# Optimization experiments

Measured on AMD Instinct MI355X. Metric: run time of the kernel, lower is better.

The kernel has to match this reference:

```python
import jax, jax.numpy as jnp
import numpy as np

EMBED = 1024

def setup_inputs() -> dict:
    key = jax.random.key(0)
    kx, kq, kk, kv = jax.random.split(key, 4)
    x = jax.random.normal(kx, (4, 2048, EMBED), dtype=jnp.float32)
    s = 1.0 / np.sqrt(EMBED)
    Wq = jax.random.normal(kq, (EMBED, EMBED), dtype=jnp.float32) * s
    Wk = jax.random.normal(kk, (EMBED, EMBED), dtype=jnp.float32) * s
    Wv = jax.random.normal(kv, (EMBED, EMBED), dtype=jnp.float32) * s
    return {"x": x, "Wq": Wq, "Wk": Wk, "Wv": Wv}

def reference(x, Wq, Wk, Wv):
    # x: [b, s, e]; nn.Linear(y) = y @ W.T, weights stored [out, in]
    Q = jnp.einsum('bse,oe->bso', x, Wq)
    K = jnp.einsum('bse,oe->bso', x, Wk)
    V = jnp.einsum('bse,oe->bso', x, Wv)
    scale = 1.0 / jnp.sqrt(jnp.asarray(x.shape[-1], x.dtype))
    energy = jnp.einsum('bqe,bke->bqk', Q, K) * scale  # [b, s, s]
    attention = jax.nn.softmax(energy, axis=-1)
    out = jnp.einsum('bqk,bke->bqe', attention, V)
    return out
```

## Files before the change

### kernel.cpp

```cpp
#include <hip/hip_runtime.h>
#include <stdint.h>


typedef __attribute__((ext_vector_type(8))) short bf16x8;
typedef __attribute__((ext_vector_type(4))) float f32x4;

__device__ __forceinline__ float bf2f(uint16_t u) {
    return __uint_as_float(((uint32_t)u) << 16);
}
__device__ __forceinline__ uint16_t f2bf(float f) {
    uint32_t u = __float_as_uint(f);
    uint32_t r = u + 0x7FFFu + ((u >> 16) & 1u);
    return (uint16_t)(r >> 16);
}

__device__ __forceinline__ void gll16(const void* g, void* l) {
    __builtin_amdgcn_global_load_lds(
        (const __attribute__((address_space(1))) uint32_t*)g,
        (__attribute__((address_space(3))) uint32_t*)l,
        16, 0, 0);
}

__global__ __launch_bounds__(256) void cast_all(const float* __restrict__ x,
                                                const float* __restrict__ Wq,
                                                const float* __restrict__ Wk,
                                                const float* __restrict__ Wv,
                                                uint16_t* __restrict__ xb,
                                                uint16_t* __restrict__ wqkvb,
                                                float* __restrict__ rowsum,
                                                int NX4, int NW4, int NZ4) {
    int i = blockIdx.x * 256 + threadIdx.x;
    const float* src;
    uint16_t* dst;
    int off;
    if (i < NX4) {
        src = x; dst = xb; off = i;
    } else {
        int j = i - NX4;
        if (j < 3 * NW4) {
            int which = j / NW4;
            off = j - which * NW4;
            src = (which == 0) ? Wq : (which == 1) ? Wk : Wv;
            dst = wqkvb + (size_t)which * NW4 * 4;
        } else {
            int z = j - 3 * NW4;
            if (z < NZ4) {
                float4 zz = {0.f, 0.f, 0.f, 0.f};
                ((float4*)rowsum)[z] = zz;
            }
            return;
        }
    }
    float4 v = ((const float4*)src)[off];
    ushort4 o;
    o.x = f2bf(v.x); o.y = f2bf(v.y); o.z = f2bf(v.z); o.w = f2bf(v.w);
    ((ushort4*)dst)[off] = o;
}

#define BK 32

template <int MODE, typename OutT>
__global__ __launch_bounds__(256) void gemm2(const uint16_t* __restrict__ A,
                                             const uint16_t* __restrict__ B,
                                             OutT* __restrict__ C,
                                             long lda, long ldb, long ldc,
                                             int K, float alpha,
                                             long sA, long sB, long sC,
                                             uint16_t* __restrict__ VtP,
                                             int vcol0,
                                             float* __restrict__ rsum) {
    const int bz = blockIdx.z;
    A += (long)bz * sA;
    B += (long)bz * sB;
    C += (long)bz * sC;

    __shared__ uint16_t As[2][128 * BK];
    __shared__ uint16_t Bs[2][128 * BK];

    const int tid  = threadIdx.x;
    const int m0   = blockIdx.y * 128;
    const int n0   = blockIdx.x * 128;
    const int wave = tid >> 6;
    const int lane = tid & 63;
    const int quad = lane >> 4;
    const int l16  = lane & 15;
    const int wr   = (wave >> 1) * 64;
    const int wc   = (wave & 1) * 64;

    const int sr = tid >> 2;
    const int sc = (tid & 3) * 8;
    const uint16_t* Ag = A + (long)(m0 + sr) * lda + sc;
    const uint16_t* Bg = B + (long)(n0 + sr) * ldb + sc;
    const long rsA = 64 * lda;
    const long rsB = 64 * ldb;
    const int so0 = sr * BK + sc;
    const int so1 = (sr + 64) * BK + sc;

    const int nk = K / BK;

    gll16(Ag,       &As[0][so0]);
    gll16(Ag + rsA, &As[0][so1]);
    gll16(Bg,       &Bs[0][so0]);
    gll16(Bg + rsB, &Bs[0][so1]);
    Ag += BK; Bg += BK;

    f32x4 acc[4][4] = {};

    for (int k = 0; k < nk; ++k) {
        const int cur = k & 1;
        __syncthreads();

        if (k + 1 < nk) {
            const int nxt = cur ^ 1;
            gll16(Ag,       &As[nxt][so0]);
            gll16(Ag + rsA, &As[nxt][so1]);
            gll16(Bg,       &Bs[nxt][so0]);
            gll16(Bg + rsB, &Bs[nxt][so1]);
            Ag += BK; Bg += BK;
        }

        const int ko = quad * 8;
        bf16x8 af[4], bfr[4];
        #pragma unroll
        for (int i = 0; i < 4; i++)
            af[i] = *(const bf16x8*)(&As[cur][(wr + i * 16 + l16) * BK + ko]);
        #pragma unroll
        for (int j = 0; j < 4; j++)
            bfr[j] = *(const bf16x8*)(&Bs[cur][(wc + j * 16 + l16) * BK + ko]);
        #pragma unroll
        for (int i = 0; i < 4; i++)
            #pragma unroll
            for (int j = 0; j < 4; j++)
                acc[i][j] = __builtin_amdgcn_mfma_f32_16x16x32_bf16(af[i], bfr[j], acc[i][j], 0, 0, 0);
    }

    if constexpr (MODE == 0) {
        if (VtP && n0 >= vcol0) {
            #pragma unroll
            for (int i = 0; i < 4; i++) {
                const int row0 = m0 + wr + i * 16 + quad * 4;
                const int b    = row0 >> 11;
                const int s    = row0 & 2047;
                #pragma unroll
                for (int j = 0; j < 4; j++) {
                    const int e = n0 + wc + j * 16 + l16 - vcol0;
                    ushort4 o;
                    o.x = f2bf(acc[i][j][0]);
                    o.y = f2bf(acc[i][j][1]);
                    o.z = f2bf(acc[i][j][2]);
                    o.w = f2bf(acc[i][j][3]);
                    *(ushort4*)(VtP + ((long)b * 1024 + e) * 2048 + s) = o;
                }
            }
        } else {
            #pragma unroll
            for (int i = 0; i < 4; i++)
                #pragma unroll
                for (int j = 0; j < 4; j++)
                    #pragma unroll
                    for (int r4 = 0; r4 < 4; r4++) {
                        int row = m0 + wr + i * 16 + quad * 4 + r4;
                        int col = n0 + wc + j * 16 + l16;
                        C[(long)row * ldc + col] = f2bf(acc[i][j][r4]);
                    }
        }
    } else if constexpr (MODE == 1) {
        float* rs = rsum + (long)bz * 2048;
        #pragma unroll
        for (int i = 0; i < 4; i++) {
            #pragma unroll
            for (int r4 = 0; r4 < 4; r4++) {
                const int row = m0 + wr + i * 16 + quad * 4 + r4;
                float part = 0.f;
                #pragma unroll
                for (int j = 0; j < 4; j++) {
                    const int col = n0 + wc + j * 16 + l16;
                    float p = __expf(acc[i][j][r4] * alpha);
                    C[(long)row * ldc + col] = f2bf(p);
                    part += p;
                }
                part += __shfl_xor(part, 1, 64);
                part += __shfl_xor(part, 2, 64);
                part += __shfl_xor(part, 4, 64);
                part += __shfl_xor(part, 8, 64);
                if (l16 == 0) atomicAdd(&rs[row], part);
            }
        }
    } else {
        const float* rs = rsum + (long)bz * 2048;
        #pragma unroll
        for (int i = 0; i < 4; i++) {
            #pragma unroll
            for (int r4 = 0; r4 < 4; r4++) {
                const int row = m0 + wr + i * 16 + quad * 4 + r4;
                const float inv = 1.0f / rs[row];
                #pragma unroll
                for (int j = 0; j < 4; j++) {
                    const int col = n0 + wc + j * 16 + l16;
                    C[(long)row * ldc + col] = acc[i][j][r4] * inv;
                }
            }
        }
    }
}

extern "C" void kernel_launch(void* const* d_in, const int* in_sizes, int n_in,
                              void* d_out, int out_size, void* d_ws, size_t ws_size,
                              hipStream_t stream) {
    const float* x  = (const float*)d_in[0];
    const float* Wq = (const float*)d_in[1];
    const float* Wk = (const float*)d_in[2];
    const float* Wv = (const float*)d_in[3];
    float* out = (float*)d_out;

    const int Bn = 4, S = 2048, E = 1024;
    const long MS = (long)Bn * S;
    const int  N3 = 3 * E;

    char* ws = (char*)d_ws;
    uint16_t* xb     = (uint16_t*)ws;  ws += (size_t)MS * E * 2;
    uint16_t* wqkvb  = (uint16_t*)ws;  ws += (size_t)N3 * E * 2;
    uint16_t* QKb    = (uint16_t*)ws;  ws += (size_t)MS * 2048 * 2;
    uint16_t* Vt     = (uint16_t*)ws;  ws += (size_t)Bn * E * S * 2;
    uint16_t* Pb     = (uint16_t*)ws;  ws += (size_t)Bn * S * S * 2;
    float*    rowsum = (float*)ws;     ws += (size_t)MS * 4;

    dim3 blk(256);

    {
        int NX4 = (int)(MS * E / 4);
        int NW4 = E * E / 4;
        int NZ4 = (int)(MS / 4);
        int tot = NX4 + 3 * NW4 + NZ4;
        cast_all<<<dim3((tot + 255) / 256), blk, 0, stream>>>(
            x, Wq, Wk, Wv, xb, wqkvb, rowsum, NX4, NW4, NZ4);
    }

    {
        dim3 g(N3 / 128, (int)(MS / 128), 1);
        gemm2<0, uint16_t><<<g, blk, 0, stream>>>(
            xb, wqkvb, QKb, E, E, 2048, E, 1.f, 0, 0, 0,
            Vt, 2048, nullptr);
    }

    {
        dim3 g(S / 128, S / 128, Bn);
        gemm2<1, uint16_t><<<g, blk, 0, stream>>>(
            QKb, QKb + 1024, Pb, 2048, 2048, S, E, 0.03125f,
            (long)S * 2048, (long)S * 2048, (long)S * S,
            nullptr, 0, rowsum);
    }

    {
        dim3 g(E / 128, S / 128, Bn);
        gemm2<2, float><<<g, blk, 0, stream>>>(
            Pb, Vt, out, S, S, E, S, 1.f,
            (long)S * S, (long)E * S, (long)S * E,
            nullptr, 0, rowsum);
    }
}
```

Before: 284.0 us.

## Swizzle QKV GEMM block order across XCDs and split Q/K into separate buffers

```diff
diff --git a/kernel.cpp b/kernel.cpp
--- a/kernel.cpp
+++ b/kernel.cpp
@@ -59,17 +59,37 @@
 
 #define BK 32
 
-template <int MODE, typename OutT>
+template <int MODE, bool SWIZ, typename OutT>
 __global__ __launch_bounds__(256) void gemm2(const uint16_t* __restrict__ A,
                                              const uint16_t* __restrict__ B,
                                              OutT* __restrict__ C,
+                                             int gx, int gy,
                                              long lda, long ldb, long ldc,
                                              int K, float alpha,
                                              long sA, long sB, long sC,
+                                             uint16_t* __restrict__ Ck,
                                              uint16_t* __restrict__ VtP,
-                                             int vcol0,
                                              float* __restrict__ rsum) {
-    const int bz = blockIdx.z;
+    int bx, by, bz;
+    if constexpr (SWIZ) {
+        const int total = gridDim.x;
+        const int nblk  = blockIdx.x;
+        const int per   = total >> 3;
+        const int g     = (nblk & 7) * per + (nblk >> 3);
+        const int pb    = gx * gy;
+        bz = g / pb;
+        const int r    = g - bz * pb;
+        const int stpr = gx >> 3;
+        const int st   = r >> 6;
+        const int w    = r & 63;
+        const int sty  = st / stpr;
+        const int stx  = st - sty * stpr;
+        bx = (stx << 3) + (w & 7);
+        by = (sty << 3) + (w >> 3);
+    } else {
+        bx = blockIdx.x; by = blockIdx.y; bz = blockIdx.z;
+    }
+
     A += (long)bz * sA;
     B += (long)bz * sB;
     C += (long)bz * sC;
@@ -78,8 +98,8 @@
     __shared__ uint16_t Bs[2][128 * BK];
 
     const int tid  = threadIdx.x;
-    const int m0   = blockIdx.y * 128;
-    const int n0   = blockIdx.x * 128;
+    const int m0   = by * 128;
+    const int n0   = bx * 128;
     const int wave = tid >> 6;
     const int lane = tid & 63;
     const int quad = lane >> 4;
@@ -135,7 +155,7 @@
     }
 
     if constexpr (MODE == 0) {
-        if (VtP && n0 >= vcol0) {
+        if (n0 >= 2048) {
             #pragma unroll
             for (int i = 0; i < 4; i++) {
                 const int row0 = m0 + wr + i * 16 + quad * 4;
@@ -143,7 +163,7 @@
                 const int s    = row0 & 2047;
                 #pragma unroll
                 for (int j = 0; j < 4; j++) {
-                    const int e = n0 + wc + j * 16 + l16 - vcol0;
+                    const int e = n0 + wc + j * 16 + l16 - 2048;
                     ushort4 o;
                     o.x = f2bf(acc[i][j][0]);
                     o.y = f2bf(acc[i][j][1]);
@@ -153,6 +173,8 @@
                 }
             }
         } else {
+            uint16_t* dst = (n0 < 1024) ? (uint16_t*)C : Ck;
+            const int coff = (n0 < 1024) ? 0 : 1024;
             #pragma unroll
             for (int i = 0; i < 4; i++)
                 #pragma unroll
@@ -160,8 +182,8 @@
                     #pragma unroll
                     for (int r4 = 0; r4 < 4; r4++) {
                         int row = m0 + wr + i * 16 + quad * 4 + r4;
-                        int col = n0 + wc + j * 16 + l16;
-                        C[(long)row * ldc + col] = f2bf(acc[i][j][r4]);
+                        int col = n0 + wc + j * 16 + l16 - coff;
+                        dst[(long)row * 1024 + col] = f2bf(acc[i][j][r4]);
                     }
         }
     } else if constexpr (MODE == 1) {
@@ -220,7 +242,8 @@
     char* ws = (char*)d_ws;
     uint16_t* xb     = (uint16_t*)ws;  ws += (size_t)MS * E * 2;
     uint16_t* wqkvb  = (uint16_t*)ws;  ws += (size_t)N3 * E * 2;
-    uint16_t* QKb    = (uint16_t*)ws;  ws += (size_t)MS * 2048 * 2;
+    uint16_t* Qb     = (uint16_t*)ws;  ws += (size_t)MS * E * 2;
+    uint16_t* Kb     = (uint16_t*)ws;  ws += (size_t)MS * E * 2;
     uint16_t* Vt     = (uint16_t*)ws;  ws += (size_t)Bn * E * S * 2;
     uint16_t* Pb     = (uint16_t*)ws;  ws += (size_t)Bn * S * S * 2;
     float*    rowsum = (float*)ws;     ws += (size_t)MS * 4;
@@ -237,25 +260,25 @@
     }
 
     {
-        dim3 g(N3 / 128, (int)(MS / 128), 1);
-        gemm2<0, uint16_t><<<g, blk, 0, stream>>>(
-            xb, wqkvb, QKb, E, E, 2048, E, 1.f, 0, 0, 0,
-            Vt, 2048, nullptr);
+        int gx = N3 / 128, gy = (int)(MS / 128);
+        gemm2<0, true, uint16_t><<<dim3(gx * gy), blk, 0, stream>>>(
+            xb, wqkvb, Qb, gx, gy, E, E, 1024, E, 1.f, 0, 0, 0,
+            Kb, Vt, nullptr);
     }
 
     {
         dim3 g(S / 128, S / 128, Bn);
-        gemm2<1, uint16_t><<<g, blk, 0, stream>>>(
-            QKb, QKb + 1024, Pb, 2048, 2048, S, E, 0.03125f,
-            (long)S * 2048, (long)S * 2048, (long)S * S,
-            nullptr, 0, rowsum);
+        gemm2<1, false, uint16_t><<<g, blk, 0, stream>>>(
+            Qb, Kb, Pb, 0, 0, E, E, S, E, 0.03125f,
+            (long)S * E, (long)S * E, (long)S * S,
+            nullptr, nullptr, rowsum);
     }
 
     {
         dim3 g(E / 128, S / 128, Bn);
-        gemm2<2, float><<<g, blk, 0, stream>>>(
-            Pb, Vt, out, S, S, E, S, 1.f,
+        gemm2<2, false, float><<<g, blk, 0, stream>>>(
+            Pb, Vt, out, 0, 0, S, S, E, S, 1.f,
             (long)S * S, (long)E * S, (long)S * E,
-            nullptr, 0, rowsum);
-    }
-}
+            nullptr, nullptr, rowsum);
+    }
+}
```

Result: faster. 276.5 us (-2.6%).
